# Optimization experiments

Measured on AMD Instinct MI355X. Metric: run time of the kernel, lower is better.

Reference implementation:

```python
import jax, jax.numpy as jnp
import numpy as np

B, S, D, K = 8, 1024, 1024, 8192


def setup_inputs() -> dict:
    key = jax.random.key(0)
    k1, k2 = jax.random.split(key)
    z = jax.random.normal(k1, (B, S, D), dtype=jnp.float32)
    codebook = jax.random.normal(k2, (K, D), dtype=jnp.float32)
    return {"z": z, "codebook": codebook}


def reference(z, codebook):
    # Eval-mode forward of VectorQuantizer (no EMA / dead-code side effects).
    b, s, d = z.shape
    z_flat = z.reshape(-1, d)                              # [N, D]
    # squared L2 distances: ||z||^2 + ||e||^2 - 2 z.e
    distances = (jnp.sum(z_flat * z_flat, axis=1, keepdims=True)
                 + jnp.sum(codebook * codebook, axis=1)
                 - 2.0 * jnp.einsum('nd,kd->nk', z_flat, codebook))  # [N, K]
    indices = jnp.argmin(distances, axis=1)                # [N]
    quantized = codebook[indices].reshape(b, s, d)         # gather
    loss = jnp.asarray(0.0, dtype=z.dtype)                 # eval mode
    # straight-through estimator
    quantized = z + jax.lax.stop_gradient(quantized - z)
    logits = -distances.reshape(b, s, -1)                  # [B, S, K]
    return quantized, indices.reshape(b, s), loss, logits
```

## Files before the change

kernel.cpp:

```cpp
#include <hip/hip_runtime.h>
#include <hip/hip_bf16.h>
#include <stdint.h>

#define NROWS 8192
#define KCODES 8192
#define DDIM 1024

#define Q_OFF    0
#define IDX_OFF  8388608
#define LOSS_OFF 8396800
#define LOG_OFF  8396801

using f32x4  = __attribute__((ext_vector_type(4))) float;
using i32x4  = __attribute__((ext_vector_type(4))) int;

__device__ __forceinline__ unsigned int forder(float f) {
  unsigned int u = __float_as_uint(f);
  return (u & 0x80000000u) ? ~u : (u | 0x80000000u);
}
__device__ __forceinline__ float finv(unsigned int u) {
  return (u & 0x80000000u) ? __uint_as_float(u & 0x7fffffffu) : __uint_as_float(~u);
}

__device__ __forceinline__ void gld_lds16(const void* g, void* l) {
  __builtin_amdgcn_global_load_lds((const __attribute__((address_space(1))) unsigned int*)g,
                                   (__attribute__((address_space(3))) unsigned int*)l,
                                   16, 0, 0);
}

__global__ __launch_bounds__(256) void vq_convert(const float* __restrict__ z,
                                                  const float* __restrict__ cb,
                                                  signed char* __restrict__ qbuf,
                                                  float* __restrict__ nrm,
                                                  float* __restrict__ scl) {
  const int r = blockIdx.x;
  const int tid = threadIdx.x;
  const float* src = (r < NROWS) ? (z + (size_t)r * DDIM)
                                 : (cb + (size_t)(r - NROWS) * DDIM);
  float4 v = reinterpret_cast<const float4*>(src)[tid];
  float vv[4] = {v.x, v.y, v.z, v.w};

  float amax = fmaxf(fmaxf(fabsf(vv[0]), fabsf(vv[1])),
                     fmaxf(fabsf(vv[2]), fabsf(vv[3])));
  float ss = vv[0]*vv[0] + vv[1]*vv[1] + vv[2]*vv[2] + vv[3]*vv[3];
  #pragma unroll
  for (int m = 32; m > 0; m >>= 1) {
    amax = fmaxf(amax, __shfl_down(amax, m, 64));
    ss += __shfl_down(ss, m, 64);
  }
  __shared__ float rA[4], rS[4], sB;
  if ((tid & 63) == 0) { rA[tid >> 6] = amax; rS[tid >> 6] = ss; }
  __syncthreads();
  if (tid == 0) {
    const float a = fmaxf(fmaxf(rA[0], rA[1]), fmaxf(rA[2], rA[3]));
    nrm[r] = rS[0] + rS[1] + rS[2] + rS[3];
    const float s = fmaxf(a, 1e-20f) * (1.0f / 127.0f);
    scl[r] = s;
    sB = s;
  }
  __syncthreads();
  const float inv = 1.0f / sB;
  int q[4];
  #pragma unroll
  for (int j = 0; j < 4; ++j) {
    int t = (int)rintf(vv[j] * inv);
    q[j] = t < -127 ? -127 : (t > 127 ? 127 : t);
  }
  const int packed = (q[0] & 255) | ((q[1] & 255) << 8) |
                     ((q[2] & 255) << 16) | (q[3] << 24);
  reinterpret_cast<int*>(qbuf + (size_t)r * DDIM)[tid] = packed;
}

__global__ __launch_bounds__(256, 4) void vq_mfma(const signed char* __restrict__ zq,
                                                  const signed char* __restrict__ cq,
                                                  const float* __restrict__ nrm,
                                                  const float* __restrict__ scl,
                                                  unsigned int* __restrict__ gmins,
                                                  float* __restrict__ out) {
  __shared__ i32x4 Asv[1024];
  __shared__ i32x4 Bsv[1024];

  const int wgid = blockIdx.x;
  const int stx = wgid & 7;
  const int idx = wgid >> 3;
  const int sty = idx >> 6;
  const int tt_ = idx & 63;
  const int bx = stx * 8 + (tt_ & 7);
  const int by = sty * 8 + (tt_ >> 3);

  const int k0 = bx * 128;
  const int n0 = by * 128;
  const int tid = threadIdx.x;
  const int wid = tid >> 6, lane = tid & 63;
  const int wm = wid >> 1, wn = wid & 1;
  const int l15 = lane & 15, l4 = lane >> 4;

  const int srow = lane >> 3;
  const int c    = lane & 7;
  const signed char* ga[4];
  const signed char* gb[4];
  int loff[4];
  #pragma unroll
  for (int q = 0; q < 4; ++q) {
    const int s = wid * 4 + q;
    const int row = s * 8 + srow;
    const int cg = c ^ (row & 7);
    ga[q] = zq + (size_t)(n0 + row) * DDIM + cg * 16;
    gb[q] = cq + (size_t)(k0 + row) * DDIM + cg * 16;
    loff[q] = s * 1024;
  }

  i32x4 acc[4][4];
  #pragma unroll
  for (int i = 0; i < 4; ++i)
    #pragma unroll
    for (int j = 0; j < 4; ++j) acc[i][j] = (i32x4){0, 0, 0, 0};

  for (int it = 0; it < 8; ++it) {
    const int d0 = it * 128;
    #pragma unroll
    for (int q = 0; q < 4; ++q) {
      gld_lds16(ga[q] + d0, (char*)Asv + loff[q]);
      gld_lds16(gb[q] + d0, (char*)Bsv + loff[q]);
    }
    __syncthreads();

    #pragma unroll
    for (int ks = 0; ks < 2; ++ks) {
      const int ch = ks * 4 + l4;
      i32x4 af[4], bf[4];
      #pragma unroll
      for (int f = 0; f < 4; ++f) {
        const int ar = wm * 64 + f * 16 + l15;
        af[f] = Asv[ar * 8 + (ch ^ (ar & 7))];
        const int br = wn * 64 + f * 16 + l15;
        bf[f] = Bsv[br * 8 + (ch ^ (br & 7))];
      }
      #pragma unroll
      for (int fm = 0; fm < 4; ++fm)
        #pragma unroll
        for (int fn = 0; fn < 4; ++fn)
          acc[fm][fn] = __builtin_amdgcn_mfma_i32_16x16x64_i8(af[fm], bf[fn], acc[fm][fn], 0, 0, 0);
    }
    __syncthreads();
  }

  float ee[4], sk[4];
  #pragma unroll
  for (int j = 0; j < 4; ++j) {
    const int kk = k0 + wn * 64 + j * 16 + l15;
    ee[j] = nrm[NROWS + kk];
    sk[j] = scl[NROWS + kk];
  }

  float* logits = out + LOG_OFF;
  #pragma unroll
  for (int f = 0; f < 4; ++f) {
    #pragma unroll
    for (int r = 0; r < 4; ++r) {
      const int n = n0 + wm * 64 + f * 16 + l4 * 4 + r;
      const float zz = nrm[n];
      const float sn2 = -2.0f * scl[n];
      float rowmin = 3.4e38f;
      #pragma unroll
      for (int j = 0; j < 4; ++j) {
        const int k = k0 + wn * 64 + j * 16 + l15;
        const float dist = fmaf(sn2 * sk[j], (float)acc[f][j][r], zz + ee[j]);
        logits[(size_t)n * KCODES + k] = -dist;
        rowmin = fminf(rowmin, dist);
      }
      #pragma unroll
      for (int mm = 1; mm < 16; mm <<= 1)
        rowmin = fminf(rowmin, __shfl_xor(rowmin, mm, 64));
      if (l15 == 0) atomicMin(&gmins[(size_t)n * 32 + (bx >> 1)], forder(rowmin));
    }
  }
}

#define MARGIN 16.0f
__global__ __launch_bounds__(256) void vq_refine(const float* __restrict__ z,
                                                 const float* __restrict__ cb,
                                                 const float* __restrict__ nrm,
                                                 const unsigned int* __restrict__ gmins,
                                                 float* __restrict__ out) {
  const int n = blockIdx.x;
  const int tid = threadIdx.x;
  __shared__ float tminS[32];
  __shared__ float gminS;
  __shared__ int cnt;
  __shared__ int cand[64];
  __shared__ float red[4];

  if (tid < 32) tminS[tid] = finv(gmins[(size_t)n * 32 + tid]);
  if (tid == 0) cnt = 0;
  __syncthreads();
  if (tid == 0) {
    float g = tminS[0];
    #pragma unroll
    for (int i = 1; i < 32; ++i) g = fminf(g, tminS[i]);
    gminS = g;
  }
  __syncthreads();
  const float thr = gminS + MARGIN;

  const float* lrow = out + LOG_OFF + (size_t)n * KCODES;
  for (int g = 0; g < 32; ++g) {
    if (tminS[g] <= thr) {
      const float dist = -lrow[g * 256 + tid];
      if (dist <= thr) {
        const int p = atomicAdd(&cnt, 1);
        if (p < 64) cand[p] = g * 256 + tid;
      }
    }
  }
  __syncthreads();
  const int ncand = min(cnt, 64);

  const float zz = nrm[n];
  const float4 zv = reinterpret_cast<const float4*>(z + (size_t)n * DDIM)[tid];
  float bestd = 0.f;
  int bestk = -1;
  for (int ci = 0; ci < ncand; ++ci) {
    const int k = cand[ci];
    const float4 ev = reinterpret_cast<const float4*>(cb + (size_t)k * DDIM)[tid];
    float s = zv.x * ev.x + zv.y * ev.y + zv.z * ev.z + zv.w * ev.w;
    #pragma unroll
    for (int mm = 32; mm > 0; mm >>= 1) s += __shfl_down(s, mm, 64);
    if ((tid & 63) == 0) red[tid >> 6] = s;
    __syncthreads();
    const float dot = red[0] + red[1] + red[2] + red[3];
    const float dist = zz + nrm[NROWS + k] - 2.0f * dot;
    if (bestk < 0 || dist < bestd || (dist == bestd && k < bestk)) {
      bestd = dist; bestk = k;
    }
    __syncthreads();
  }

  const float4* src = reinterpret_cast<const float4*>(cb + (size_t)bestk * DDIM);
  float4* dst = reinterpret_cast<float4*>(out + (size_t)n * DDIM);
  dst[tid] = src[tid];
  if (tid == 0) {
    out[IDX_OFF + n] = (float)bestk;
    if (n == 0) out[LOSS_OFF] = 0.f;
  }
}

extern "C" void kernel_launch(void* const* d_in, const int* in_sizes, int n_in,
                              void* d_out, int out_size, void* d_ws, size_t ws_size,
                              hipStream_t stream) {
  const float* z  = (const float*)d_in[0];
  const float* cb = (const float*)d_in[1];
  float* out = (float*)d_out;

  float* nrm = (float*)d_ws;
  float* scl = (float*)((char*)d_ws + 65536);
  unsigned int* gmins = (unsigned int*)((char*)d_ws + 131072);

  signed char* qbuf = (signed char*)out;
  const signed char* zq = qbuf;
  const signed char* cq = qbuf + (size_t)NROWS * DDIM;

  hipMemsetAsync((char*)d_ws + 131072, 0xFF, (size_t)NROWS * 32 * 4, stream);
  vq_convert<<<NROWS + KCODES, 256, 0, stream>>>(z, cb, qbuf, nrm, scl);
  vq_mfma<<<4096, 256, 0, stream>>>(zq, cq, nrm, scl, gmins, out);
  vq_refine<<<NROWS, 256, 0, stream>>>(z, cb, nrm, gmins, out);
}
```

Measured before the change: 208.2 us.

## Double-buffer int8 MFMA K-loop and fold gmins init into convert kernel

Replaces the single-buffered 128-wide K-step loop with a double-buffered 64-wide pipeline. The next tile's global-to-LDS loads are issued before the current tile's MFMAs run, with a new swizzle and s_setprio around the MFMA block. This is meant to hide load latency and drop one of the two barriers per iteration. It also removes the separate hipMemset by having the first 1024 blocks of the convert kernel initialise gmins, saving one launch. In exchange the loop takes twice as many barrier iterations, and the correctness of the new swizzle and buffering needs care.

```diff
diff --git a/kernel.cpp b/kernel.cpp
--- a/kernel.cpp
+++ b/kernel.cpp
@@ -32,9 +32,12 @@
                                                   const float* __restrict__ cb,
                                                   signed char* __restrict__ qbuf,
                                                   float* __restrict__ nrm,
-                                                  float* __restrict__ scl) {
+                                                  float* __restrict__ scl,
+                                                  unsigned int* __restrict__ gmins) {
   const int r = blockIdx.x;
   const int tid = threadIdx.x;
+  if (r < 1024) gmins[r * 256 + tid] = 0xFFFFFFFFu;
+
   const float* src = (r < NROWS) ? (z + (size_t)r * DDIM)
                                  : (cb + (size_t)(r - NROWS) * DDIM);
   float4 v = reinterpret_cast<const float4*>(src)[tid];
@@ -77,8 +80,7 @@
                                                   const float* __restrict__ scl,
                                                   unsigned int* __restrict__ gmins,
                                                   float* __restrict__ out) {
-  __shared__ i32x4 Asv[1024];
-  __shared__ i32x4 Bsv[1024];
+  __shared__ i32x4 lds[2048];
 
   const int wgid = blockIdx.x;
   const int stx = wgid & 7;
@@ -95,20 +97,28 @@
   const int wm = wid >> 1, wn = wid & 1;
   const int l15 = lane & 15, l4 = lane >> 4;
 
-  const int srow = lane >> 3;
-  const int c    = lane & 7;
-  const signed char* ga[4];
-  const signed char* gb[4];
-  int loff[4];
-  #pragma unroll
-  for (int q = 0; q < 4; ++q) {
-    const int s = wid * 4 + q;
-    const int row = s * 8 + srow;
-    const int cg = c ^ (row & 7);
+  const signed char* ga[2];
+  const signed char* gb[2];
+  int ldst[2];
+  #pragma unroll
+  for (int q = 0; q < 2; ++q) {
+    const int s = wid * 2 + q;
+    const int row = s * 16 + (lane >> 2);
+    const int cg = (lane & 3) ^ ((row >> 1) & 3);
     ga[q] = zq + (size_t)(n0 + row) * DDIM + cg * 16;
     gb[q] = cq + (size_t)(k0 + row) * DDIM + cg * 16;
-    loff[q] = s * 1024;
-  }
+    ldst[q] = s * 1024;
+  }
+
+  auto stage = [&](int t, int b) {
+    const int d0 = t * 64;
+    #pragma unroll
+    for (int q = 0; q < 2; ++q)
+      gld_lds16(ga[q] + d0, (char*)lds + b * 16384 + ldst[q]);
+    #pragma unroll
+    for (int q = 0; q < 2; ++q)
+      gld_lds16(gb[q] + d0, (char*)lds + b * 16384 + 8192 + ldst[q]);
+  };
 
   i32x4 acc[4][4];
   #pragma unroll
@@ -116,33 +126,36 @@
     #pragma unroll
     for (int j = 0; j < 4; ++j) acc[i][j] = (i32x4){0, 0, 0, 0};
 
-  for (int it = 0; it < 8; ++it) {
-    const int d0 = it * 128;
-    #pragma unroll
-    for (int q = 0; q < 4; ++q) {
-      gld_lds16(ga[q] + d0, (char*)Asv + loff[q]);
-      gld_lds16(gb[q] + d0, (char*)Bsv + loff[q]);
-    }
-    __syncthreads();
-
-    #pragma unroll
-    for (int ks = 0; ks < 2; ++ks) {
-      const int ch = ks * 4 + l4;
-      i32x4 af[4], bf[4];
+  stage(0, 0);
+  asm volatile("s_waitcnt vmcnt(0)" ::: "memory");
+  __builtin_amdgcn_s_barrier();
+
+  #pragma unroll 2
+  for (int t = 0; t < 16; ++t) {
+    const int cur = t & 1;
+    if (t < 15) stage(t + 1, cur ^ 1);
+    const int base = cur * 1024;
+    i32x4 af[4], bf[4];
+    #pragma unroll
+    for (int f = 0; f < 4; ++f) {
+      const int ar = wm * 64 + f * 16 + l15;
+      af[f] = lds[base + ar * 4 + (l4 ^ ((ar >> 1) & 3))];
+      const int br = wn * 64 + f * 16 + l15;
+      bf[f] = lds[base + 512 + br * 4 + (l4 ^ ((br >> 1) & 3))];
+    }
+    asm volatile("s_waitcnt lgkmcnt(0)" ::: "memory");
+    __builtin_amdgcn_sched_barrier(0);
+    __builtin_amdgcn_s_setprio(1);
+    #pragma unroll
+    for (int fm = 0; fm < 4; ++fm)
       #pragma unroll
-      for (int f = 0; f < 4; ++f) {
-        const int ar = wm * 64 + f * 16 + l15;
-        af[f] = Asv[ar * 8 + (ch ^ (ar & 7))];
-        const int br = wn * 64 + f * 16 + l15;
-        bf[f] = Bsv[br * 8 + (ch ^ (br & 7))];
-      }
-      #pragma unroll
-      for (int fm = 0; fm < 4; ++fm)
-        #pragma unroll
-        for (int fn = 0; fn < 4; ++fn)
-          acc[fm][fn] = __builtin_amdgcn_mfma_i32_16x16x64_i8(af[fm], bf[fn], acc[fm][fn], 0, 0, 0);
-    }
-    __syncthreads();
+      for (int fn = 0; fn < 4; ++fn)
+        acc[fm][fn] = __builtin_amdgcn_mfma_i32_16x16x64_i8(af[fm], bf[fn], acc[fm][fn], 0, 0, 0);
+    __builtin_amdgcn_s_setprio(0);
+    if (t < 15) {
+      asm volatile("s_waitcnt vmcnt(0)" ::: "memory");
+      __builtin_amdgcn_s_barrier();
+    }
   }
 
   float ee[4], sk[4];
@@ -260,8 +273,7 @@
   const signed char* zq = qbuf;
   const signed char* cq = qbuf + (size_t)NROWS * DDIM;
 
-  hipMemsetAsync((char*)d_ws + 131072, 0xFF, (size_t)NROWS * 32 * 4, stream);
-  vq_convert<<<NROWS + KCODES, 256, 0, stream>>>(z, cb, qbuf, nrm, scl);
+  vq_convert<<<NROWS + KCODES, 256, 0, stream>>>(z, cb, qbuf, nrm, scl, gmins);
   vq_mfma<<<4096, 256, 0, stream>>>(zq, cq, nrm, scl, gmins, out);
   vq_refine<<<NROWS, 256, 0, stream>>>(z, cb, nrm, gmins, out);
 }
```

After: 202.1 us, median of 2. -3.0%, faster.
